# Optimization experiments

Hardware: AMD Instinct MI355X
Metric: run time of the kernel (lower is better)

The kernel has to match this reference:

```python
import jax, jax.numpy as jnp
import numpy as np

B, S, H, F, E, K, NS = 2, 2048, 2048, 768, 32, 4, 8
SZ = F // NS  # secondary expert size (96)
CAP = 2 * (B * S) * K // E


def setup_inputs() -> dict:
    key = jax.random.key(0)
    k = jax.random.split(key, 7)
    s = 0.02
    return {
        "router_input": jax.random.normal(k[0], (B, S, H), jnp.float32),
        "hidden_states": jax.random.normal(k[1], (B, S, H), jnp.float32),
        "w_router": jax.random.normal(k[2], (H, E), jnp.float32) * s,
        "w_up": jax.random.normal(k[3], (E, H, F), jnp.float32) * s,
        "w_gate": jax.random.normal(k[4], (E, H, F), jnp.float32) * s,
        "w_down": jax.random.normal(k[5], (E, F, H), jnp.float32) * s,
        "w_sgate": jax.random.normal(k[6], (E, H, NS), jnp.float32) * s,
    }


def reference(router_input, hidden_states, w_router, w_up, w_gate, w_down, w_sgate):
    b, s, h = hidden_states.shape
    x = hidden_states.reshape(-1, h)          # [T,H]
    r = router_input.reshape(-1, h)           # [T,H] (early router input)
    T = x.shape[0]

    # top-k routing (early router, softmax over top-k logits)
    logits = r @ w_router                     # [T,E]
    top_logits, sel = jax.lax.top_k(logits, K)  # [T,K]
    rw = jax.nn.softmax(top_logits.astype(jnp.float32), axis=-1).astype(x.dtype)

    # combined per-(expert, token) routing weight and hit mask
    onehot = jax.nn.one_hot(sel, E, dtype=x.dtype)      # [T,K,E]
    wmat = (onehot * rw[..., None]).sum(1).T            # [E,T]
    mask = onehot.sum(1).T                              # [E,T] in {0,1}

    # fixed-capacity dispatch: per expert gather up to CAP routed tokens
    valid, idx = jax.lax.top_k(mask, CAP)               # [E,CAP]
    w = jnp.take_along_axis(wmat, idx, axis=1) * valid  # [E,CAP]

    xe = x[idx]                                         # [E,CAP,H]
    re = r[idx]                                         # [E,CAP,H]

    # hierarchical MLP: secondary gate (hard sigmoid>0.5) over NS groups
    sg = (jax.nn.sigmoid(jnp.einsum('ech,ehs->ecs', re, w_sgate)) > 0.5).astype(x.dtype)
    act = jnp.einsum('ech,ehf->ecf', xe, w_up) * jax.nn.relu(jnp.einsum('ech,ehf->ecf', xe, w_gate))
    act = (act.reshape(E, CAP, NS, SZ) * sg[..., None]).reshape(E, CAP, F)
    out = jnp.einsum('ecf,efh->ech', act, w_down) * w[..., None]  # weighted combine

    # scatter-accumulate back to tokens (invalid slots have zero weight)
    final = jnp.zeros((T, h), x.dtype).at[idx.reshape(-1)].add(out.reshape(-1, h))
    return final.reshape(b, s, h), top_logits
```

## Files before the change

kernel.cpp:

```cpp
#include <hip/hip_runtime.h>

#define TT 4096
#define HD 2048
#define FD 768
#define NE 32
#define TOPK 4
#define NSG 8
#define CAPE 1024
#define MAXTILES 160
#define UPGRID (MAXTILES * 6)
#define DNGRID (MAXTILES * 16)

typedef __attribute__((ext_vector_type(8))) short short8;
typedef __attribute__((ext_vector_type(4))) float f32x4;
typedef __attribute__((ext_vector_type(4))) unsigned short us4;
typedef __attribute__((ext_vector_type(8))) unsigned short us8;

__device__ __forceinline__ unsigned short f2bf(float f) {
  unsigned u = __builtin_bit_cast(unsigned, f);
  u += 0x7FFFu + ((u >> 16) & 1u);
  return (unsigned short)(u >> 16);
}

__device__ __forceinline__ void async16(const void* g, void* l) {
  __builtin_amdgcn_global_load_lds(
      (const __attribute__((address_space(1))) unsigned int*)g,
      (__attribute__((address_space(3))) unsigned int*)l, 16, 0, 0);
}

__global__ __launch_bounds__(256) void wrt_kernel(const float* __restrict__ w_router,
                                                  float* __restrict__ wrt) {
  int idx = blockIdx.x * 256 + threadIdx.x;
  int e = idx >> 11, h = idx & 2047;
  wrt[idx] = w_router[h * NE + e];
}

#define LSTR 68
__global__ __launch_bounds__(256) void logits_kernel(
    const float* __restrict__ rin, const float* __restrict__ wrt,
    float* __restrict__ logits) {
  __shared__ float As[16 * LSTR];
  __shared__ float Bs[32 * LSTR];
  const int tid = threadIdx.x;
  const int t0 = blockIdx.x * 16;
  const int tp = tid >> 4, eg = tid & 15;
  f32x4 acc0 = (f32x4)0.f, acc1 = (f32x4)0.f;
  for (int kt = 0; kt < HD; kt += 64) {
    __syncthreads();
    {
      int row = tid >> 4, col = (tid & 15) * 4;
      *(f32x4*)&As[row * LSTR + col] =
          *(const f32x4*)&rin[(size_t)(t0 + row) * HD + kt + col];
    }
    {
      int e = tid >> 3, col = (tid & 7) * 8;
      *(f32x4*)&Bs[e * LSTR + col] = *(const f32x4*)&wrt[(size_t)e * HD + kt + col];
      *(f32x4*)&Bs[e * LSTR + col + 4] =
          *(const f32x4*)&wrt[(size_t)e * HD + kt + col + 4];
    }
    __syncthreads();
#pragma unroll
    for (int k4 = 0; k4 < 16; ++k4) {
      f32x4 a = *(const f32x4*)&As[tp * LSTR + k4 * 4];
      f32x4 b0 = *(const f32x4*)&Bs[eg * LSTR + k4 * 4];
      f32x4 b1 = *(const f32x4*)&Bs[(eg + 16) * LSTR + k4 * 4];
      acc0 += a * b0;
      acc1 += a * b1;
    }
  }
  logits[(t0 + tp) * NE + eg] = acc0[0] + acc0[1] + acc0[2] + acc0[3];
  logits[(t0 + tp) * NE + eg + 16] = acc1[0] + acc1[1] + acc1[2] + acc1[3];
}

__global__ __launch_bounds__(256) void topk_kernel(
    const float* __restrict__ logits, float* __restrict__ top_logits,
    int* __restrict__ sel, float* __restrict__ rwts) {
  __shared__ float lg[256 * 33];
  const int tid = threadIdx.x;
  const int t0 = blockIdx.x * 256;
#pragma unroll
  for (int i = 0; i < 8; ++i) {
    int fi = tid + i * 256;
    f32x4 v = *(const f32x4*)&logits[(size_t)t0 * NE + fi * 4];
    int tok = fi >> 3, e0 = (fi & 7) * 4;
#pragma unroll
    for (int c = 0; c < 4; ++c) lg[tok * 33 + e0 + c] = v[c];
  }
  __syncthreads();
  const float* row = &lg[tid * 33];
  float val[TOPK];
  int idx[TOPK];
  unsigned used = 0;
#pragma unroll
  for (int k = 0; k < TOPK; ++k) {
    float best = -1e30f;
    int bi = 0;
    for (int e = 0; e < NE; ++e) {
      float v = row[e];
      if (!((used >> e) & 1u) && v > best) { best = v; bi = e; }
    }
    used |= 1u << bi;
    val[k] = best;
    idx[k] = bi;
  }
  float ex[TOPK], sum = 0.f;
#pragma unroll
  for (int k = 0; k < TOPK; ++k) { ex[k] = expf(val[k] - val[0]); sum += ex[k]; }
  int t = t0 + tid;
#pragma unroll
  for (int k = 0; k < TOPK; ++k) {
    top_logits[t * TOPK + k] = val[k];
    sel[t * TOPK + k] = idx[k];
    rwts[t * TOPK + k] = ex[k] / sum;
  }
}

__global__ __launch_bounds__(256) void dispatch_kernel(
    const int* __restrict__ sel, const float* __restrict__ rwts,
    int* __restrict__ tok_idx, float* __restrict__ tok_w, int* __restrict__ counts) {
  const int e = blockIdx.x;
  __shared__ int wcnt[4];
  __shared__ int base;
  const int tid = threadIdx.x, lane = tid & 63, wid = tid >> 6;
  if (tid == 0) base = 0;
  __syncthreads();
  for (int t0 = 0; t0 < TT; t0 += 256) {
    int t = t0 + tid;
    int hitk = -1;
#pragma unroll
    for (int k = 0; k < TOPK; ++k)
      if (sel[t * TOPK + k] == e) hitk = k;
    unsigned long long m = __ballot(hitk >= 0);
    if (lane == 0) wcnt[wid] = __popcll(m);
    __syncthreads();
    int off = base;
    for (int w = 0; w < wid; ++w) off += wcnt[w];
    int pos = off + __popcll(m & ((1ULL << lane) - 1ULL));
    if (hitk >= 0 && pos < CAPE) {
      tok_idx[e * CAPE + pos] = t;
      tok_w[e * CAPE + pos] = rwts[t * TOPK + hitk];
    }
    __syncthreads();
    if (tid == 0) base += wcnt[0] + wcnt[1] + wcnt[2] + wcnt[3];
    __syncthreads();
  }
  if (tid == 0) counts[e] = base < CAPE ? base : CAPE;
}

__global__ void build_tiles_kernel(const int* __restrict__ counts,
                                   int* __restrict__ tlist, int* __restrict__ ntiles) {
  if (threadIdx.x == 0) {
    int n = 0;
    for (int e = 0; e < NE; ++e) {
      int c = counts[e];
      int mb = (c + 127) >> 7;
      for (int m = 0; m < mb; ++m) tlist[n++] = (e << 8) | m;
    }
    ntiles[0] = n;
  }
}

__global__ __launch_bounds__(256) void sgate_kernel(
    const float* __restrict__ rin, const float* __restrict__ w_sgate,
    const int* __restrict__ tok_idx, const int* __restrict__ counts,
    unsigned* __restrict__ sgbits) {
  const int e = blockIdx.y;
  const int count = counts[e];
  const int s0 = blockIdx.x * 128;
  if (s0 >= count || count == 0) return;
  __shared__ float wsgS[2048 * 9];
  const int tid = threadIdx.x, lane = tid & 63, wid = tid >> 6;
  const float* wsg = w_sgate + (size_t)e * (HD * NSG);
#pragma unroll
  for (int p = 0; p < 8; ++p) {
    int row = p * 256 + tid;
    f32x4 v0 = *(const f32x4*)&wsg[row * 8];
    f32x4 v1 = *(const f32x4*)&wsg[row * 8 + 4];
#pragma unroll
    for (int c = 0; c < 4; ++c) {
      wsgS[row * 9 + c] = v0[c];
      wsgS[row * 9 + 4 + c] = v1[c];
    }
  }
  __syncthreads();
  const int base = s0 + wid * 32;
  for (int j = 0; j < 16; ++j) {
    int sA = base + j, sB = base + j + 16;
    if (sA >= count) break;
    int tokA = tok_idx[e * CAPE + sA];
    int tokB = tok_idx[e * CAPE + (sB < count ? sB : sA)];
    float zA[8], zB[8];
#pragma unroll
    for (int s = 0; s < 8; ++s) { zA[s] = 0.f; zB[s] = 0.f; }
    const float* rAp = rin + (size_t)tokA * HD;
    const float* rBp = rin + (size_t)tokB * HD;
#pragma unroll 4
    for (int i = 0; i < 32; ++i) {
      int h = lane + 64 * i;
      float rA = rAp[h];
      float rB = rBp[h];
#pragma unroll
      for (int s = 0; s < 8; ++s) {
        float w = wsgS[h * 9 + s];
        zA[s] += rA * w;
        zB[s] += rB * w;
      }
    }
#pragma unroll
    for (int s = 0; s < 8; ++s) {
#pragma unroll
      for (int d = 1; d < 64; d <<= 1) {
        zA[s] += __shfl_xor(zA[s], d);
        zB[s] += __shfl_xor(zB[s], d);
      }
    }
    if (lane == 0) {
      unsigned bA = 0, bB = 0;
#pragma unroll
      for (int s = 0; s < 8; ++s) {
        bA |= ((unsigned)(zA[s] > 0.f)) << s;
        bB |= ((unsigned)(zB[s] > 0.f)) << s;
      }
      sgbits[e * CAPE + sA] = bA;
      if (sB < count) sgbits[e * CAPE + sB] = bB;
    }
  }
}

__global__ __launch_bounds__(256) void cvt_x_kernel(const float* __restrict__ x,
                                                    unsigned short* __restrict__ xb) {
  size_t i = ((size_t)blockIdx.x * 256 + threadIdx.x) * 8;
  float4 a = *(const float4*)(x + i);
  float4 b = *(const float4*)(x + i + 4);
  us8 o = {f2bf(a.x), f2bf(a.y), f2bf(a.z), f2bf(a.w),
           f2bf(b.x), f2bf(b.y), f2bf(b.z), f2bf(b.w)};
  *(us8*)(xb + i) = o;
}

__global__ __launch_bounds__(256) void transpose_cvt_kernel(
    const float* __restrict__ in, unsigned short* __restrict__ out, int R, int C) {
  const int e = blockIdx.z;
  const int r0 = blockIdx.x * 64, c0 = blockIdx.y * 64;
  __shared__ float t[64][65];
  const int tid = threadIdx.x;
  const float* inp = in + (size_t)e * R * C;
  {
    const int row = tid >> 4, col4 = (tid & 15) << 2;
#pragma unroll
    for (int p = 0; p < 4; ++p) {
      float4 v = *(const float4*)(inp + (size_t)(r0 + p * 16 + row) * C + c0 + col4);
      t[p * 16 + row][col4 + 0] = v.x;
      t[p * 16 + row][col4 + 1] = v.y;
      t[p * 16 + row][col4 + 2] = v.z;
      t[p * 16 + row][col4 + 3] = v.w;
    }
  }
  __syncthreads();
  {
    const int c = tid >> 2, j = tid & 3;
    us8 o0, o1;
#pragma unroll
    for (int i = 0; i < 8; ++i) o0[i] = f2bf(t[j * 16 + i][c]);
#pragma unroll
    for (int i = 0; i < 8; ++i) o1[i] = f2bf(t[j * 16 + 8 + i][c]);
    unsigned short* op = out + (size_t)e * R * C + (size_t)(c0 + c) * R + r0 + j * 16;
    *(us8*)op = o0;
    *(us8*)(op + 8) = o1;
  }
}

__global__ __launch_bounds__(256, 2) void up_gate_bf16(
    const unsigned short* __restrict__ xb, const unsigned short* __restrict__ wub,
    const unsigned short* __restrict__ wgb, const int* __restrict__ tok_idx,
    const int* __restrict__ counts, const unsigned* __restrict__ sgbits,
    const int* __restrict__ tlist, const int* __restrict__ ntiles,
    unsigned short* __restrict__ act) {
  const int hw = blockIdx.x;
  const int idx = (hw & 7) * (UPGRID / 8) + (hw >> 3);
  const int ti = idx / 6, nb = idx - ti * 6;
  if (ti >= ntiles[0]) return;
  const int entry = tlist[ti];
  const int e = entry >> 8;
  const int m0 = (entry & 255) << 7;
  const int n0 = nb * 128;
  const int count = counts[e];

  __shared__ __align__(16) unsigned short As[128 * 64];
  __shared__ __align__(16) unsigned short Bu[128 * 64];
  __shared__ __align__(16) unsigned short Bg[128 * 64];

  const int tid = threadIdx.x, lane = tid & 63, wid = tid >> 6;
  const int wr = wid >> 1, wc = wid & 1;
  const int ecap = e * CAPE;

  const int srow = tid >> 3, sblk = tid & 7;
  const unsigned short *gA[4], *gU[4], *gG[4];
#pragma unroll
  for (int c = 0; c < 4; ++c) {
    int r = c * 32 + srow;
    int gm = m0 + r;
    int gc = gm < count ? gm : count - 1;
    int swz = (sblk ^ (r & 7)) << 3;
    gA[c] = xb + (size_t)tok_idx[ecap + gc] * HD + swz;
    gU[c] = wub + (size_t)(e * FD + n0 + r) * HD + swz;
    gG[c] = wgb + (size_t)(e * FD + n0 + r) * HD + swz;
  }
  unsigned short* lA = As + (tid << 3);
  unsigned short* lU = Bu + (tid << 3);
  unsigned short* lG = Bg + (tid << 3);

  f32x4 accU[4][4], accG[4][4];
#pragma unroll
  for (int i = 0; i < 4; ++i)
#pragma unroll
    for (int j = 0; j < 4; ++j) { accU[i][j] = (f32x4)0.f; accG[i][j] = (f32x4)0.f; }

  const int fr = lane & 15, fq = lane >> 4;
  const int frx = (fr & 7) << 3;

  for (int kt = 0; kt < HD; kt += 64) {
    __syncthreads();
#pragma unroll
    for (int c = 0; c < 4; ++c) {
      async16(gA[c] + kt, lA + c * 2048);
      async16(gU[c] + kt, lU + c * 2048);
      async16(gG[c] + kt, lG + c * 2048);
    }
    __syncthreads();
#pragma unroll
    for (int kk = 0; kk < 64; kk += 32) {
      short8 af[4], bu[4], bg[4];
      const int kphys = (kk + fq * 8) ^ frx;
#pragma unroll
      for (int mi = 0; mi < 4; ++mi)
        af[mi] = *(const short8*)(As + ((wr * 64 + mi * 16 + fr) << 6) + kphys);
#pragma unroll
      for (int ni = 0; ni < 4; ++ni) {
        bu[ni] = *(const short8*)(Bu + ((wc * 64 + ni * 16 + fr) << 6) + kphys);
        bg[ni] = *(const short8*)(Bg + ((wc * 64 + ni * 16 + fr) << 6) + kphys);
      }
#pragma unroll
      for (int mi = 0; mi < 4; ++mi)
#pragma unroll
        for (int ni = 0; ni < 4; ++ni) {
          accU[mi][ni] = __builtin_amdgcn_mfma_f32_16x16x32_bf16(af[mi], bu[ni], accU[mi][ni], 0, 0, 0);
          accG[mi][ni] = __builtin_amdgcn_mfma_f32_16x16x32_bf16(af[mi], bg[ni], accG[mi][ni], 0, 0, 0);
        }
    }
  }
#pragma unroll
  for (int mi = 0; mi < 4; ++mi) {
#pragma unroll
    for (int q = 0; q < 4; ++q) {
      int grow = m0 + wr * 64 + mi * 16 + fq * 4 + q;
      if (grow < count) {
        unsigned sg = sgbits[ecap + grow];
        unsigned short* arow = act + (size_t)(ecap + grow) * FD + n0 + wc * 64 + fr;
#pragma unroll
        for (int ni = 0; ni < 4; ++ni) {
          int gcol = n0 + wc * 64 + ni * 16 + fr;
          float a = accU[mi][ni][q] * fmaxf(accG[mi][ni][q], 0.f);
          a = ((sg >> (gcol / 96)) & 1u) ? a : 0.f;
          arow[ni * 16] = f2bf(a);
        }
      }
    }
  }
}

__global__ __launch_bounds__(256, 3) void down_bf16(
    const unsigned short* __restrict__ act, const unsigned short* __restrict__ wdb,
    const int* __restrict__ tok_idx, const float* __restrict__ tok_w,
    const int* __restrict__ counts, const int* __restrict__ tlist,
    const int* __restrict__ ntiles, float* __restrict__ outF) {
  const int hw = blockIdx.x;
  const int idx = (hw & 7) * (DNGRID / 8) + (hw >> 3);
  const int ti = idx >> 4, nb = idx & 15;
  if (ti >= ntiles[0]) return;
  const int entry = tlist[ti];
  const int e = entry >> 8;
  const int m0 = (entry & 255) << 7;
  const int n0 = nb * 128;
  const int count = counts[e];

  __shared__ __align__(16) unsigned short As[128 * 64];
  __shared__ __align__(16) unsigned short Bs[128 * 64];

  const int tid = threadIdx.x, lane = tid & 63, wid = tid >> 6;
  const int wr = wid >> 1, wc = wid & 1;
  const int ecap = e * CAPE;

  const int srow = tid >> 3, sblk = tid & 7;
  const unsigned short *gA[4], *gB[4];
#pragma unroll
  for (int c = 0; c < 4; ++c) {
    int r = c * 32 + srow;
    int gr = m0 + r;
    if (gr > CAPE - 1) gr = CAPE - 1;
    int swz = (sblk ^ (r & 7)) << 3;
    gA[c] = act + (size_t)(ecap + gr) * FD + swz;
    gB[c] = wdb + (size_t)(e * HD + n0 + r) * FD + swz;
  }
  unsigned short* lA = As + (tid << 3);
  unsigned short* lB = Bs + (tid << 3);

  f32x4 accD[4][4];
#pragma unroll
  for (int i = 0; i < 4; ++i)
#pragma unroll
    for (int j = 0; j < 4; ++j) accD[i][j] = (f32x4)0.f;

  const int fr = lane & 15, fq = lane >> 4;
  const int frx = (fr & 7) << 3;

  for (int kt = 0; kt < FD; kt += 64) {
    __syncthreads();
#pragma unroll
    for (int c = 0; c < 4; ++c) {
      async16(gA[c] + kt, lA + c * 2048);
      async16(gB[c] + kt, lB + c * 2048);
    }
    __syncthreads();
#pragma unroll
    for (int kk = 0; kk < 64; kk += 32) {
      short8 af[4], bb[4];
      const int kphys = (kk + fq * 8) ^ frx;
#pragma unroll
      for (int mi = 0; mi < 4; ++mi)
        af[mi] = *(const short8*)(As + ((wr * 64 + mi * 16 + fr) << 6) + kphys);
#pragma unroll
      for (int ni = 0; ni < 4; ++ni)
        bb[ni] = *(const short8*)(Bs + ((wc * 64 + ni * 16 + fr) << 6) + kphys);
#pragma unroll
      for (int mi = 0; mi < 4; ++mi)
#pragma unroll
        for (int ni = 0; ni < 4; ++ni)
          accD[mi][ni] = __builtin_amdgcn_mfma_f32_16x16x32_bf16(af[mi], bb[ni], accD[mi][ni], 0, 0, 0);
    }
  }
#pragma unroll
  for (int mi = 0; mi < 4; ++mi) {
#pragma unroll
    for (int q = 0; q < 4; ++q) {
      int grow = m0 + wr * 64 + mi * 16 + fq * 4 + q;
      if (grow < count) {
        float wgt = tok_w[ecap + grow];
        float* dst = outF + (size_t)tok_idx[ecap + grow] * HD + n0 + wc * 64 + fr;
#pragma unroll
        for (int ni = 0; ni < 4; ++ni)
          atomicAdd(dst + ni * 16, accD[mi][ni][q] * wgt);
      }
    }
  }
}

extern "C" void kernel_launch(void* const* d_in, const int* in_sizes, int n_in,
                              void* d_out, int out_size, void* d_ws, size_t ws_size,
                              hipStream_t stream) {
  const float* rin = (const float*)d_in[0];
  const float* x = (const float*)d_in[1];
  const float* w_router = (const float*)d_in[2];
  const float* w_up = (const float*)d_in[3];
  const float* w_gate = (const float*)d_in[4];
  const float* w_down = (const float*)d_in[5];
  const float* w_sg = (const float*)d_in[6];
  float* outF = (float*)d_out;
  float* top_logits = outF + (size_t)TT * HD;

  char* ws = (char*)d_ws;
  int* sel = (int*)(ws + 0);
  float* rwts = (float*)(ws + (64 << 10));
  int* tidx = (int*)(ws + (192 << 10));
  float* tw = (float*)(ws + (320 << 10));
  unsigned* sgb = (unsigned*)(ws + (448 << 10));
  int* counts = (int*)(ws + (576 << 10));
  int* tlist = (int*)(ws + (580 << 10));
  int* ntiles = (int*)(ws + (584 << 10));
  float* logits = (float*)(ws + (640 << 10));
  unsigned short* act = (unsigned short*)(ws + ((size_t)2 << 20));
  float* wrt = (float*)(ws + ((size_t)51 << 20));
  unsigned short* xb = (unsigned short*)(ws + ((size_t)52 << 20));
  unsigned short* wub = (unsigned short*)(ws + ((size_t)69 << 20));
  unsigned short* wgb = wub + (size_t)NE * HD * FD;
  unsigned short* wdb = wgb + (size_t)NE * HD * FD;

  hipMemsetAsync(d_out, 0, (size_t)TT * HD * sizeof(float), stream);

  wrt_kernel<<<256, 256, 0, stream>>>(w_router, wrt);
  logits_kernel<<<TT / 16, 256, 0, stream>>>(rin, wrt, logits);
  topk_kernel<<<TT / 256, 256, 0, stream>>>(logits, top_logits, sel, rwts);
  dispatch_kernel<<<NE, 256, 0, stream>>>(sel, rwts, tidx, tw, counts);
  build_tiles_kernel<<<1, 64, 0, stream>>>(counts, tlist, ntiles);
  sgate_kernel<<<dim3(CAPE / 128, NE), 256, 0, stream>>>(rin, w_sg, tidx, counts, sgb);

  cvt_x_kernel<<<(TT * HD) / (256 * 8), 256, 0, stream>>>(x, xb);
  transpose_cvt_kernel<<<dim3(HD / 64, FD / 64, NE), 256, 0, stream>>>(w_up, wub, HD, FD);
  transpose_cvt_kernel<<<dim3(HD / 64, FD / 64, NE), 256, 0, stream>>>(w_gate, wgb, HD, FD);
  transpose_cvt_kernel<<<dim3(FD / 64, HD / 64, NE), 256, 0, stream>>>(w_down, wdb, FD, HD);

  up_gate_bf16<<<UPGRID, 256, 0, stream>>>(xb, wub, wgb, tidx, counts, sgb, tlist, ntiles, act);
  down_bf16<<<DNGRID, 256, 0, stream>>>(act, wdb, tidx, tw, counts, tlist, ntiles, outF);
}
```

Baseline: 621.4 us.

## Replace atomic scatter with bf16 staging plus combine kernel; narrow up-gate tiles

The down GEMM now writes its per-slot results to a bf16 staging buffer, which reuses the converted up-weight region, instead of scattering fp32 atomics into the output. A new combine kernel gathers each token's up to four slots through a slot map built during dispatch and applies the routing weights. This removes the output memset and the atomic contention, at the cost of an extra read and write of roughly 128MB and bf16 rounding of the down outputs. Separately, the up/gate kernel uses 64-wide N tiles with higher occupancy, giving twice as many blocks and fewer registers per block.

```diff
diff --git a/kernel.cpp b/kernel.cpp
--- a/kernel.cpp
+++ b/kernel.cpp
@@ -8,7 +8,7 @@
 #define NSG 8
 #define CAPE 1024
 #define MAXTILES 160
-#define UPGRID (MAXTILES * 6)
+#define UPGRID (MAXTILES * 12)
 #define DNGRID (MAXTILES * 16)
 
 typedef __attribute__((ext_vector_type(8))) short short8;
@@ -20,6 +20,9 @@
   unsigned u = __builtin_bit_cast(unsigned, f);
   u += 0x7FFFu + ((u >> 16) & 1u);
   return (unsigned short)(u >> 16);
+}
+__device__ __forceinline__ float bf2f(unsigned short b) {
+  return __builtin_bit_cast(float, (unsigned)b << 16);
 }
 
 __device__ __forceinline__ void async16(const void* g, void* l) {
@@ -117,7 +120,8 @@
 
 __global__ __launch_bounds__(256) void dispatch_kernel(
     const int* __restrict__ sel, const float* __restrict__ rwts,
-    int* __restrict__ tok_idx, float* __restrict__ tok_w, int* __restrict__ counts) {
+    int* __restrict__ tok_idx, float* __restrict__ tok_w, int* __restrict__ counts,
+    int* __restrict__ slotmap) {
   const int e = blockIdx.x;
   __shared__ int wcnt[4];
   __shared__ int base;
@@ -136,9 +140,14 @@
     int off = base;
     for (int w = 0; w < wid; ++w) off += wcnt[w];
     int pos = off + __popcll(m & ((1ULL << lane) - 1ULL));
-    if (hitk >= 0 && pos < CAPE) {
-      tok_idx[e * CAPE + pos] = t;
-      tok_w[e * CAPE + pos] = rwts[t * TOPK + hitk];
+    if (hitk >= 0) {
+      if (pos < CAPE) {
+        tok_idx[e * CAPE + pos] = t;
+        tok_w[e * CAPE + pos] = rwts[t * TOPK + hitk];
+        slotmap[t * TOPK + hitk] = e * CAPE + pos;
+      } else {
+        slotmap[t * TOPK + hitk] = -1;
+      }
     }
     __syncthreads();
     if (tid == 0) base += wcnt[0] + wcnt[1] + wcnt[2] + wcnt[3];
@@ -269,7 +278,7 @@
   }
 }
 
-__global__ __launch_bounds__(256, 2) void up_gate_bf16(
+__global__ __launch_bounds__(256, 3) void up_gate_bf16(
     const unsigned short* __restrict__ xb, const unsigned short* __restrict__ wub,
     const unsigned short* __restrict__ wgb, const int* __restrict__ tok_idx,
     const int* __restrict__ counts, const unsigned* __restrict__ sgbits,
@@ -277,24 +286,24 @@
     unsigned short* __restrict__ act) {
   const int hw = blockIdx.x;
   const int idx = (hw & 7) * (UPGRID / 8) + (hw >> 3);
-  const int ti = idx / 6, nb = idx - ti * 6;
+  const int ti = idx / 12, nb = idx - ti * 12;
   if (ti >= ntiles[0]) return;
   const int entry = tlist[ti];
   const int e = entry >> 8;
   const int m0 = (entry & 255) << 7;
-  const int n0 = nb * 128;
+  const int n0 = nb * 64;
   const int count = counts[e];
 
   __shared__ __align__(16) unsigned short As[128 * 64];
-  __shared__ __align__(16) unsigned short Bu[128 * 64];
-  __shared__ __align__(16) unsigned short Bg[128 * 64];
+  __shared__ __align__(16) unsigned short Bu[64 * 64];
+  __shared__ __align__(16) unsigned short Bg[64 * 64];
 
   const int tid = threadIdx.x, lane = tid & 63, wid = tid >> 6;
   const int wr = wid >> 1, wc = wid & 1;
   const int ecap = e * CAPE;
 
   const int srow = tid >> 3, sblk = tid & 7;
-  const unsigned short *gA[4], *gU[4], *gG[4];
+  const unsigned short *gA[4], *gU[2], *gG[2];
 #pragma unroll
   for (int c = 0; c < 4; ++c) {
     int r = c * 32 + srow;
@@ -302,6 +311,11 @@
     int gc = gm < count ? gm : count - 1;
     int swz = (sblk ^ (r & 7)) << 3;
     gA[c] = xb + (size_t)tok_idx[ecap + gc] * HD + swz;
+  }
+#pragma unroll
+  for (int c = 0; c < 2; ++c) {
+    int r = c * 32 + srow;
+    int swz = (sblk ^ (r & 7)) << 3;
     gU[c] = wub + (size_t)(e * FD + n0 + r) * HD + swz;
     gG[c] = wgb + (size_t)(e * FD + n0 + r) * HD + swz;
   }
@@ -309,11 +323,11 @@
   unsigned short* lU = Bu + (tid << 3);
   unsigned short* lG = Bg + (tid << 3);
 
-  f32x4 accU[4][4], accG[4][4];
+  f32x4 accU[4][2], accG[4][2];
 #pragma unroll
   for (int i = 0; i < 4; ++i)
 #pragma unroll
-    for (int j = 0; j < 4; ++j) { accU[i][j] = (f32x4)0.f; accG[i][j] = (f32x4)0.f; }
+    for (int j = 0; j < 2; ++j) { accU[i][j] = (f32x4)0.f; accG[i][j] = (f32x4)0.f; }
 
   const int fr = lane & 15, fq = lane >> 4;
   const int frx = (fr & 7) << 3;
@@ -321,28 +335,29 @@
   for (int kt = 0; kt < HD; kt += 64) {
     __syncthreads();
 #pragma unroll
-    for (int c = 0; c < 4; ++c) {
-      async16(gA[c] + kt, lA + c * 2048);
+    for (int c = 0; c < 4; ++c) async16(gA[c] + kt, lA + c * 2048);
+#pragma unroll
+    for (int c = 0; c < 2; ++c) {
       async16(gU[c] + kt, lU + c * 2048);
       async16(gG[c] + kt, lG + c * 2048);
     }
     __syncthreads();
 #pragma unroll
     for (int kk = 0; kk < 64; kk += 32) {
-      short8 af[4], bu[4], bg[4];
+      short8 af[4], bu[2], bg[2];
       const int kphys = (kk + fq * 8) ^ frx;
 #pragma unroll
       for (int mi = 0; mi < 4; ++mi)
         af[mi] = *(const short8*)(As + ((wr * 64 + mi * 16 + fr) << 6) + kphys);
 #pragma unroll
-      for (int ni = 0; ni < 4; ++ni) {
-        bu[ni] = *(const short8*)(Bu + ((wc * 64 + ni * 16 + fr) << 6) + kphys);
-        bg[ni] = *(const short8*)(Bg + ((wc * 64 + ni * 16 + fr) << 6) + kphys);
+      for (int ni = 0; ni < 2; ++ni) {
+        bu[ni] = *(const short8*)(Bu + ((wc * 32 + ni * 16 + fr) << 6) + kphys);
+        bg[ni] = *(const short8*)(Bg + ((wc * 32 + ni * 16 + fr) << 6) + kphys);
       }
 #pragma unroll
       for (int mi = 0; mi < 4; ++mi)
 #pragma unroll
-        for (int ni = 0; ni < 4; ++ni) {
+        for (int ni = 0; ni < 2; ++ni) {
           accU[mi][ni] = __builtin_amdgcn_mfma_f32_16x16x32_bf16(af[mi], bu[ni], accU[mi][ni], 0, 0, 0);
           accG[mi][ni] = __builtin_amdgcn_mfma_f32_16x16x32_bf16(af[mi], bg[ni], accG[mi][ni], 0, 0, 0);
         }
@@ -355,10 +370,10 @@
       int grow = m0 + wr * 64 + mi * 16 + fq * 4 + q;
       if (grow < count) {
         unsigned sg = sgbits[ecap + grow];
-        unsigned short* arow = act + (size_t)(ecap + grow) * FD + n0 + wc * 64 + fr;
-#pragma unroll
-        for (int ni = 0; ni < 4; ++ni) {
-          int gcol = n0 + wc * 64 + ni * 16 + fr;
+        unsigned short* arow = act + (size_t)(ecap + grow) * FD + n0 + wc * 32 + fr;
+#pragma unroll
+        for (int ni = 0; ni < 2; ++ni) {
+          int gcol = n0 + wc * 32 + ni * 16 + fr;
           float a = accU[mi][ni][q] * fmaxf(accG[mi][ni][q], 0.f);
           a = ((sg >> (gcol / 96)) & 1u) ? a : 0.f;
           arow[ni * 16] = f2bf(a);
@@ -370,9 +385,8 @@
 
 __global__ __launch_bounds__(256, 3) void down_bf16(
     const unsigned short* __restrict__ act, const unsigned short* __restrict__ wdb,
-    const int* __restrict__ tok_idx, const float* __restrict__ tok_w,
     const int* __restrict__ counts, const int* __restrict__ tlist,
-    const int* __restrict__ ntiles, float* __restrict__ outF) {
+    const int* __restrict__ ntiles, unsigned short* __restrict__ act_dn) {
   const int hw = blockIdx.x;
   const int idx = (hw & 7) * (DNGRID / 8) + (hw >> 3);
   const int ti = idx >> 4, nb = idx & 15;
@@ -444,14 +458,40 @@
     for (int q = 0; q < 4; ++q) {
       int grow = m0 + wr * 64 + mi * 16 + fq * 4 + q;
       if (grow < count) {
-        float wgt = tok_w[ecap + grow];
-        float* dst = outF + (size_t)tok_idx[ecap + grow] * HD + n0 + wc * 64 + fr;
+        unsigned short* drow = act_dn + (size_t)(ecap + grow) * HD + n0 + wc * 64 + fr;
 #pragma unroll
         for (int ni = 0; ni < 4; ++ni)
-          atomicAdd(dst + ni * 16, accD[mi][ni][q] * wgt);
-      }
-    }
-  }
+          drow[ni * 16] = f2bf(accD[mi][ni][q]);
+      }
+    }
+  }
+}
+
+__global__ __launch_bounds__(256) void combine_kernel(
+    const unsigned short* __restrict__ act_dn, const float* __restrict__ tok_w,
+    const int* __restrict__ slotmap, float* __restrict__ outF) {
+  const int t = blockIdx.x;
+  const int h = threadIdx.x * 8;
+  const int4 sm = *(const int4*)(slotmap + t * TOPK);
+  float acc[8];
+#pragma unroll
+  for (int j = 0; j < 8; ++j) acc[j] = 0.f;
+  const int ss[4] = {sm.x, sm.y, sm.z, sm.w};
+#pragma unroll
+  for (int k = 0; k < TOPK; ++k) {
+    int s = ss[k];
+    if (s >= 0) {
+      float w = tok_w[s];
+      us8 v = *(const us8*)(act_dn + (size_t)s * HD + h);
+#pragma unroll
+      for (int j = 0; j < 8; ++j) acc[j] += w * bf2f(v[j]);
+    }
+  }
+  float* op = outF + (size_t)t * HD + h;
+  f32x4 o0 = {acc[0], acc[1], acc[2], acc[3]};
+  f32x4 o1 = {acc[4], acc[5], acc[6], acc[7]};
+  *(f32x4*)op = o0;
+  *(f32x4*)(op + 4) = o1;
 }
 
 extern "C" void kernel_launch(void* const* d_in, const int* in_sizes, int n_in,
@@ -477,19 +517,19 @@
   int* tlist = (int*)(ws + (580 << 10));
   int* ntiles = (int*)(ws + (584 << 10));
   float* logits = (float*)(ws + (640 << 10));
+  int* slotmap = (int*)(ws + (1152 << 10));
   unsigned short* act = (unsigned short*)(ws + ((size_t)2 << 20));
   float* wrt = (float*)(ws + ((size_t)51 << 20));
   unsigned short* xb = (unsigned short*)(ws + ((size_t)52 << 20));
   unsigned short* wub = (unsigned short*)(ws + ((size_t)69 << 20));
   unsigned short* wgb = wub + (size_t)NE * HD * FD;
   unsigned short* wdb = wgb + (size_t)NE * HD * FD;
-
-  hipMemsetAsync(d_out, 0, (size_t)TT * HD * sizeof(float), stream);
+  unsigned short* act_dn = wub;
 
   wrt_kernel<<<256, 256, 0, stream>>>(w_router, wrt);
   logits_kernel<<<TT / 16, 256, 0, stream>>>(rin, wrt, logits);
   topk_kernel<<<TT / 256, 256, 0, stream>>>(logits, top_logits, sel, rwts);
-  dispatch_kernel<<<NE, 256, 0, stream>>>(sel, rwts, tidx, tw, counts);
+  dispatch_kernel<<<NE, 256, 0, stream>>>(sel, rwts, tidx, tw, counts, slotmap);
   build_tiles_kernel<<<1, 64, 0, stream>>>(counts, tlist, ntiles);
   sgate_kernel<<<dim3(CAPE / 128, NE), 256, 0, stream>>>(rin, w_sg, tidx, counts, sgb);
 
@@ -499,5 +539,6 @@
   transpose_cvt_kernel<<<dim3(FD / 64, HD / 64, NE), 256, 0, stream>>>(w_down, wdb, FD, HD);
 
   up_gate_bf16<<<UPGRID, 256, 0, stream>>>(xb, wub, wgb, tidx, counts, sgb, tlist, ntiles, act);
-  down_bf16<<<DNGRID, 256, 0, stream>>>(act, wdb, tidx, tw, counts, tlist, ntiles, outF);
-}
+  down_bf16<<<DNGRID, 256, 0, stream>>>(act, wdb, counts, tlist, ntiles, act_dn);
+  combine_kernel<<<TT, 256, 0, stream>>>(act_dn, tw, slotmap, outF);
+}
```

Result: faster. 574.0 us (-7.6%).
